# Performance work log

Hardware: AMD Instinct MI355X
Metric: run time of the kernel (lower is better)

The kernel has to match this reference:

```python
import jax, jax.numpy as jnp
import numpy as np


def _binarize(w):
    # sign(w) with sign(0) mapped to +1, matching the torch forward
    return jnp.where(w >= 0, 1.0, -1.0).astype(w.dtype)


def setup_inputs() -> dict:
    key = jax.random.key(0)
    k1, k2, k3 = jax.random.split(key, 3)
    N, IN, OUT = 8192, 4096, 4096
    x = jax.random.normal(k1, (N, IN), dtype=jnp.float32)
    weight = jax.random.normal(k2, (OUT, IN), dtype=jnp.float32)
    fan_in = IN
    bound = 1.0 / fan_in ** 0.5
    bias = jax.random.uniform(k3, (OUT,), dtype=jnp.float32, minval=-bound, maxval=bound)
    return {"x": x, "weight": weight, "bias": bias}


def reference(x, weight, bias):
    # forward: clamp(-1,1) then sign-binarize; clamp does not change the sign,
    # so binarized weight is simply sign(weight) with 0 -> +1.
    w_clamped = jnp.clip(weight, -1.0, 1.0)
    bw = _binarize(w_clamped)  # [OUT, IN] of +/-1
    # F.linear: x @ W^T + b
    return jnp.einsum('ni,oi->no', x, bw) + bias
```

## Files before the change

### kernel.cpp

```cpp
#include <hip/hip_runtime.h>
#include <stdint.h>

#define M_DIM 8192
#define N_DIM 4096
#define K_DIM 4096
#define NT    (K_DIM / 128)

typedef __attribute__((ext_vector_type(4))) int int32x4;

#define QUANT_BLOCKS 2048
#define SIGN_BLOCKS  1024
#define SIGN_THREADS (SIGN_BLOCKS * 256)

__global__ __launch_bounds__(256) void prep_kernel(const float* __restrict__ x,
                                                   const float* __restrict__ w,
                                                   signed char* __restrict__ xq,
                                                   signed char* __restrict__ wq,
                                                   float* __restrict__ scales) {
  const int bid = blockIdx.x;
  const int t = threadIdx.x;
  if (bid < QUANT_BLOCKS) {
    const int wave = t >> 6, lane = t & 63;
    const int row = bid * 4 + wave;
    const float4* xr = (const float4*)(x + (size_t)row * K_DIM);
    float4 v[16];
    float amax = 0.f;
#pragma unroll
    for (int j = 0; j < 16; j++) {
      v[j] = xr[lane + 64 * j];
      amax = fmaxf(amax, fmaxf(fmaxf(fabsf(v[j].x), fabsf(v[j].y)),
                               fmaxf(fabsf(v[j].z), fabsf(v[j].w))));
    }
#pragma unroll
    for (int off = 32; off > 0; off >>= 1)
      amax = fmaxf(amax, __shfl_xor(amax, off, 64));
    amax = fmaxf(amax, 1e-30f);
    const float rsc = 127.0f / amax;
    if (lane == 0) scales[row] = amax / 127.0f;
    int* qr = (int*)(xq + (size_t)row * K_DIM);
#pragma unroll
    for (int j = 0; j < 16; j++) {
      int q0 = __float2int_rn(v[j].x * rsc);
      int q1 = __float2int_rn(v[j].y * rsc);
      int q2 = __float2int_rn(v[j].z * rsc);
      int q3 = __float2int_rn(v[j].w * rsc);
      qr[lane + 64 * j] = (q0 & 255) | ((q1 & 255) << 8) | ((q2 & 255) << 16) | (q3 << 24);
    }
  } else {
    const int idx0 = (bid - QUANT_BLOCKS) * 256 + t;
    const float4* wf = (const float4*)w;
    int4* o = (int4*)wq;
#pragma unroll
    for (int k = 0; k < 4; k++) {
      const int idx = idx0 + k * SIGN_THREADS;
      int4 pk;
      int* pi = (int*)&pk;
#pragma unroll
      for (int j = 0; j < 4; j++) {
        float4 a = wf[(size_t)idx * 4 + j];
        unsigned b0 = a.x >= 0.f ? 0x01u : 0xFFu;
        unsigned b1 = a.y >= 0.f ? 0x01u : 0xFFu;
        unsigned b2 = a.z >= 0.f ? 0x01u : 0xFFu;
        unsigned b3 = a.w >= 0.f ? 0x01u : 0xFFu;
        pi[j] = (int)(b0 | (b1 << 8) | (b2 << 16) | (b3 << 24));
      }
      o[idx] = pk;
    }
  }
}

__device__ __forceinline__ void async16(const signed char* g, signed char* l) {
  __builtin_amdgcn_global_load_lds((const __attribute__((address_space(1))) void*)g,
                                   (__attribute__((address_space(3))) void*)l, 16, 0, 0);
}


#define STAGE_A(b, h, k0)                                                      \
  do {                                                                         \
    async16(gA + (h) * (128L * K_DIM) + (k0),                                  \
            &lds[(b) * 32768 + (h) * 16384 + wave * 1024]);                    \
    async16(gA + (h) * (128L * K_DIM) + 64L * K_DIM + (k0),                    \
            &lds[(b) * 32768 + (h) * 16384 + 8192 + wave * 1024]);             \
  } while (0)

#define STAGE_B(b, h, k0)                                                      \
  do {                                                                         \
    async16(gB + (h) * (128L * K_DIM) + (k0),                                  \
            &lds[65536 + (b) * 32768 + (h) * 16384 + wave * 1024]);            \
    async16(gB + (h) * (128L * K_DIM) + 64L * K_DIM + (k0),                    \
            &lds[65536 + (b) * 32768 + (h) * 16384 + 8192 + wave * 1024]);     \
  } while (0)

#define PHASE(BUF, Q, STAGE_STMT, TAIL_STMT)                                   \
  {                                                                            \
    int32x4 af[2][2];                                                          \
    _Pragma("unroll") for (int kk = 0; kk < 2; ++kk)                           \
    _Pragma("unroll") for (int i2 = 0; i2 < 2; ++i2)                           \
      af[i2][kk] = *(const int32x4*)&lds[(BUF) * 32768 + aoff[kk] +            \
                                         (2 * (Q) + i2) * 2048];               \
    STAGE_STMT;                                                                \
    __builtin_amdgcn_s_barrier();                                              \
    __builtin_amdgcn_s_setprio(1);                                             \
    _Pragma("unroll") for (int kk = 0; kk < 2; ++kk)                           \
    _Pragma("unroll") for (int i2 = 0; i2 < 2; ++i2)                           \
    _Pragma("unroll") for (int fj = 0; fj < 4; ++fj)                           \
      acc[2 * (Q) + i2][fj] = __builtin_amdgcn_mfma_i32_16x16x64_i8(           \
          af[i2][kk], bfr[fj][kk], acc[2 * (Q) + i2][fj], 0, 0, 0);            \
    __builtin_amdgcn_s_setprio(0);                                             \
    TAIL_STMT;                                                                 \
    __builtin_amdgcn_s_barrier();                                              \
  }

#define WINDOW(BUF, KA, KB)                                                    \
  {                                                                            \
    int32x4 bfr[4][2];                                                         \
    _Pragma("unroll") for (int kk = 0; kk < 2; ++kk)                           \
    _Pragma("unroll") for (int fj = 0; fj < 4; ++fj)                           \
      bfr[fj][kk] =                                                            \
          *(const int32x4*)&lds[(BUF) * 32768 + boff[kk] + fj * 2048];         \
    PHASE(BUF, 0, STAGE_A(1 - (BUF), 0, KA), (void)0)                          \
    PHASE(BUF, 1, STAGE_A(1 - (BUF), 1, KA), (void)0)                          \
    PHASE(BUF, 2, STAGE_B(BUF, 0, KB), (void)0)                                \
    PHASE(BUF, 3, STAGE_B(BUF, 1, KB),                                         \
          asm volatile("s_waitcnt vmcnt(4)" ::: "memory"))                     \
  }

__global__ __launch_bounds__(512, 2) void gemm_i8_kernel(
    const signed char* __restrict__ A,
    const signed char* __restrict__ B,
    const float* __restrict__ scales,
    const float* __restrict__ bias,
    float* __restrict__ C) {
  __shared__ __align__(16) signed char lds[131072];

  const int tid  = threadIdx.x;
  const int wave = tid >> 6;
  const int lane = tid & 63;
  const int wm = wave >> 2;
  const int wn = wave & 3;
  const int qd = lane >> 4, l16 = lane & 15;

  int wg = blockIdx.x;
  wg = (wg & 7) * (512 / 8) + (wg >> 3);
  const int bx = wg & 15;
  const int by = wg >> 4;
  const long m0 = (long)by * 256;
  const long n0 = (long)bx * 256;

  const int roff = tid >> 3;
  const int poff = ((tid & 7) ^ ((tid >> 3) & 7)) << 4;
  const signed char* gA = A + (m0 + roff) * K_DIM + poff;
  const signed char* gB = B + (n0 + roff) * K_DIM + poff;

  const int swz = l16 & 7;
  int aoff[2], boff[2];
#pragma unroll
  for (int kk = 0; kk < 2; ++kk) {
    const int pp = ((kk * 4 + qd) ^ swz) << 4;
    aoff[kk] = (wm * 128 + l16) * 128 + pp;
    boff[kk] = 65536 + (wn * 64 + l16) * 128 + pp;
  }

  int32x4 acc[8][4];
#pragma unroll
  for (int i = 0; i < 8; ++i)
#pragma unroll
    for (int j = 0; j < 4; ++j)
      acc[i][j] = (int32x4){0, 0, 0, 0};

  STAGE_A(0, 0, 0);
  STAGE_A(0, 1, 0);
  STAGE_B(0, 0, 0);
  STAGE_B(0, 1, 0);
  STAGE_B(1, 0, 128);
  STAGE_B(1, 1, 128);
  asm volatile("s_waitcnt vmcnt(4)" ::: "memory");
  __builtin_amdgcn_s_barrier();

#pragma unroll 1
  for (int W = 0; W < NT; W += 2) {
    const long kA0 = (long)((W + 1 < NT) ? (W + 1) : (NT - 1)) * 128;
    const long kB0 = (long)((W + 2 < NT) ? (W + 2) : (NT - 1)) * 128;
    WINDOW(0, kA0, kB0)
    const long kA1 = (long)((W + 2 < NT) ? (W + 2) : (NT - 1)) * 128;
    const long kB1 = (long)((W + 3 < NT) ? (W + 3) : (NT - 1)) * 128;
    WINDOW(1, kA1, kB1)
  }

  asm volatile("s_waitcnt vmcnt(0)" ::: "memory");
  __builtin_amdgcn_s_barrier();

  const long row0 = m0 + wm * 128 + qd * 4;
  const long col0 = n0 + wn * 64 + l16;
#pragma unroll
  for (int fj = 0; fj < 4; ++fj) {
    const float bv = bias[col0 + fj * 16];
#pragma unroll
    for (int fi = 0; fi < 8; ++fi) {
      const long r = row0 + fi * 16;
      float4 sv = *(const float4*)&scales[r];
      const float* s = &sv.x;
#pragma unroll
      for (int i = 0; i < 4; ++i) {
        C[(r + i) * N_DIM + col0 + fj * 16] = (float)acc[fi][fj][i] * s[i] + bv;
      }
    }
  }
}

extern "C" void kernel_launch(void* const* d_in, const int* in_sizes, int n_in,
                              void* d_out, int out_size, void* d_ws, size_t ws_size,
                              hipStream_t stream) {
  const float* x    = (const float*)d_in[0];
  const float* w    = (const float*)d_in[1];
  const float* bias = (const float*)d_in[2];
  float* out = (float*)d_out;

  signed char* xq = (signed char*)d_ws;
  signed char* wq = xq + (size_t)M_DIM * K_DIM;
  float* scales   = (float*)(wq + (size_t)N_DIM * K_DIM);

  prep_kernel<<<QUANT_BLOCKS + SIGN_BLOCKS, 256, 0, stream>>>(x, w, xq, wq, scales);

  gemm_i8_kernel<<<dim3((M_DIM / 256) * (N_DIM / 256)), dim3(512), 0, stream>>>(
      xq, wq, scales, bias, out);
}
```

Measured before the change: 391.4 us.

## Collapse per-phase barriers into two per window and prefetch A fragments

Restructures the inner K-window of the int8 MFMA GEMM so it no longer runs four phases with two barriers each. A fragments for two quarter-tiles are loaded up front and the later ones are loaded one step ahead. The async stages are issued between MFMA groups, with only two workgroup barriers per window. The aim is to cut barrier stalls and let LDS reads overlap MFMA work, at the cost of more live VGPRs for the extra fragment buffers.

```diff
diff --git a/kernel.cpp b/kernel.cpp
--- a/kernel.cpp
+++ b/kernel.cpp
@@ -91,25 +91,24 @@
             &lds[65536 + (b) * 32768 + (h) * 16384 + 8192 + wave * 1024]);     \
   } while (0)
 
-#define PHASE(BUF, Q, STAGE_STMT, TAIL_STMT)                                   \
-  {                                                                            \
-    int32x4 af[2][2];                                                          \
+#define LOAD_AF(DST, BUF, Q)                                                   \
+  do {                                                                         \
     _Pragma("unroll") for (int kk = 0; kk < 2; ++kk)                           \
     _Pragma("unroll") for (int i2 = 0; i2 < 2; ++i2)                           \
-      af[i2][kk] = *(const int32x4*)&lds[(BUF) * 32768 + aoff[kk] +            \
-                                         (2 * (Q) + i2) * 2048];               \
-    STAGE_STMT;                                                                \
-    __builtin_amdgcn_s_barrier();                                              \
+      DST[i2][kk] = *(const int32x4*)&lds[(BUF) * 32768 + aoff[kk] +           \
+                                          (2 * (Q) + i2) * 2048];              \
+  } while (0)
+
+#define MFMA_Q(Q, AF)                                                          \
+  do {                                                                         \
     __builtin_amdgcn_s_setprio(1);                                             \
     _Pragma("unroll") for (int kk = 0; kk < 2; ++kk)                           \
     _Pragma("unroll") for (int i2 = 0; i2 < 2; ++i2)                           \
     _Pragma("unroll") for (int fj = 0; fj < 4; ++fj)                           \
       acc[2 * (Q) + i2][fj] = __builtin_amdgcn_mfma_i32_16x16x64_i8(           \
-          af[i2][kk], bfr[fj][kk], acc[2 * (Q) + i2][fj], 0, 0, 0);            \
+          AF[i2][kk], bfr[fj][kk], acc[2 * (Q) + i2][fj], 0, 0, 0);            \
     __builtin_amdgcn_s_setprio(0);                                             \
-    TAIL_STMT;                                                                 \
-    __builtin_amdgcn_s_barrier();                                              \
-  }
+  } while (0)
 
 #define WINDOW(BUF, KA, KB)                                                    \
   {                                                                            \
@@ -118,11 +117,22 @@
     _Pragma("unroll") for (int fj = 0; fj < 4; ++fj)                           \
       bfr[fj][kk] =                                                            \
           *(const int32x4*)&lds[(BUF) * 32768 + boff[kk] + fj * 2048];         \
-    PHASE(BUF, 0, STAGE_A(1 - (BUF), 0, KA), (void)0)                          \
-    PHASE(BUF, 1, STAGE_A(1 - (BUF), 1, KA), (void)0)                          \
-    PHASE(BUF, 2, STAGE_B(BUF, 0, KB), (void)0)                                \
-    PHASE(BUF, 3, STAGE_B(BUF, 1, KB),                                         \
-          asm volatile("s_waitcnt vmcnt(4)" ::: "memory"))                     \
+    int32x4 af0[2][2], af1[2][2], af2[2][2], af3[2][2];                        \
+    LOAD_AF(af0, BUF, 0);                                                      \
+    LOAD_AF(af1, BUF, 1);                                                      \
+    STAGE_A(1 - (BUF), 0, KA);                                                 \
+    STAGE_A(1 - (BUF), 1, KA);                                                 \
+    MFMA_Q(0, af0);                                                            \
+    __builtin_amdgcn_s_barrier();                                              \
+    LOAD_AF(af2, BUF, 2);                                                      \
+    STAGE_B(BUF, 0, KB);                                                       \
+    MFMA_Q(1, af1);                                                            \
+    LOAD_AF(af3, BUF, 3);                                                      \
+    STAGE_B(BUF, 1, KB);                                                       \
+    MFMA_Q(2, af2);                                                            \
+    MFMA_Q(3, af3);                                                            \
+    asm volatile("s_waitcnt vmcnt(4)" ::: "memory");                           \
+    __builtin_amdgcn_s_barrier();                                              \
   }
 
 __global__ __launch_bounds__(512, 2) void gemm_i8_kernel(
```

Result: no change. 391.9 us (+0.1%).
